# Kernel optimization log

Hardware: AMD Instinct MI355X
Metric: run time of the kernel (lower is better)

## Reference

```python
import jax, jax.numpy as jnp
import numpy as np

N_NODES = 50000


def _gcn_norm(edge_index, num_nodes):
    # PyG gcn_norm with add_self_loops=True, edge_weight=1
    loops = jnp.arange(num_nodes, dtype=edge_index.dtype)
    src = jnp.concatenate([edge_index[0], loops])
    dst = jnp.concatenate([edge_index[1], loops])
    deg = jax.ops.segment_sum(jnp.ones_like(dst, dtype=jnp.float32), dst,
                              num_segments=num_nodes)
    deg_inv_sqrt = jnp.where(deg > 0, jax.lax.rsqrt(jnp.maximum(deg, 1.0)), 0.0)
    norm = deg_inv_sqrt[src] * deg_inv_sqrt[dst]  # [E + N]
    return src, dst, norm


def _gcn_conv(x, src, dst, norm, W, b, num_nodes):
    h = x @ W                                 # [N, out] dense transform first
    msg = h[src] * norm[:, None]              # gather + scale, [E+N, out]
    out = jax.ops.segment_sum(msg, dst, num_segments=num_nodes)  # scatter-add
    return out + b


def setup_inputs() -> dict:
    key = jax.random.key(0)
    k1, k2, k3, k4, k5 = jax.random.split(key, 5)
    in_ch, out_ch = 128, 64
    hid = 2 * out_ch
    x = jax.random.normal(k1, (N_NODES, in_ch), dtype=jnp.float32)
    edge_index = jax.random.randint(k2, (2, 800000), 0, N_NODES, dtype=jnp.int64)
    # Glorot init like PyG GCNConv
    W1 = jax.random.normal(k3, (in_ch, hid), dtype=jnp.float32) * (1.0 / np.sqrt(in_ch))
    b1 = jnp.zeros((hid,), dtype=jnp.float32)
    W2 = jax.random.normal(k4, (hid, out_ch), dtype=jnp.float32) * (1.0 / np.sqrt(hid))
    b2 = jnp.zeros((out_ch,), dtype=jnp.float32)
    return {"x": x, "edge_index": edge_index, "W1": W1, "b1": b1,
            "W2": W2, "b2": b2}


def reference(x, edge_index, W1, b1, W2, b2):
    num_nodes = x.shape[0]
    src, dst, norm = _gcn_norm(edge_index, num_nodes)
    h = _gcn_conv(x, src, dst, norm, W1, b1, num_nodes)
    h = jax.nn.relu(h)
    return _gcn_conv(h, src, dst, norm, W2, b2, num_nodes)
```

## Files before the change

kernel.cpp:

```cpp
#include <hip/hip_runtime.h>

#define N_NODES 50000
#define N_EDGES 800000
#define IN_CH   128
#define HID     128
#define OUT_CH  64

#define NBUCK 196
#define BCAP  5120
#define XPAD  136

#define G1_BLOCKS ((N_NODES + 63) / 64)
#define GSPLIT 391

typedef __attribute__((ext_vector_type(8))) short bf16x8;
typedef __attribute__((ext_vector_type(4))) float f32x4;
typedef unsigned short ushort_t;

__device__ __forceinline__ unsigned short f2bf(float f) {
    unsigned u = __float_as_uint(f);
    u += 0x7fffu + ((u >> 16) & 1u);
    return (unsigned short)(u >> 16);
}
__device__ __forceinline__ unsigned pack2(float a, float b) {
    return (unsigned)f2bf(a) | ((unsigned)f2bf(b) << 16);
}
__device__ __forceinline__ float bf_lo(unsigned u) { return __uint_as_float(u << 16); }
__device__ __forceinline__ float bf_hi(unsigned u) { return __uint_as_float(u & 0xffff0000u); }


__global__ __launch_bounds__(256) void k_prep(const float* __restrict__ W1,
                                              const float* __restrict__ W2,
                                              ushort_t* __restrict__ W1t,
                                              ushort_t* __restrict__ W2t,
                                              int* __restrict__ bcur) {
    if (blockIdx.x == 0 && threadIdx.x < NBUCK) bcur[threadIdx.x] = 0;
    int i = blockIdx.x * 256 + threadIdx.x;
    if (i < 128 * 128) {
        int k = i >> 7, c = i & 127;
        W1t[c * 128 + k] = f2bf(W1[k * 128 + c]);
    } else {
        int j = i - 128 * 128;
        if (j < 128 * 64) {
            int k = j >> 6, c = j & 63;
            W2t[c * 128 + k] = f2bf(W2[k * 64 + c]);
        }
    }
}


__global__ __launch_bounds__(256) void k_stage(const int phase, const int tile0,
                                               const int* __restrict__ src,
                                               const int* __restrict__ dst,
                                               int* __restrict__ bcur,
                                               unsigned* __restrict__ rec,
                                               const float* __restrict__ x,
                                               const ushort_t* __restrict__ W1t,
                                               ushort_t* __restrict__ g,
                                               int* __restrict__ row_beg,
                                               int* __restrict__ row_end,
                                               float* __restrict__ dis,
                                               int* __restrict__ col) {
    __shared__ char smem[52224];
    const int tid = threadIdx.x;

    if (blockIdx.x < NBUCK) {
        if (phase == 0) {
            int* cnt  = (int*)smem;
            int* boff = cnt + 256;
            int* gdel = boff + 256;
            int* bid  = gdel + 256;
            unsigned* stage = (unsigned*)(bid + 4096);

            const int base = blockIdx.x * 4096;
            const int nval = min(4096, N_EDGES - base);

            int dreg[16];
#pragma unroll
            for (int k = 0; k < 16; ++k) {
                int e = base + k * 256 + tid;
                dreg[k] = (e < N_EDGES) ? dst[e] : -1;
            }
            cnt[tid] = 0;
            __syncthreads();
#pragma unroll
            for (int k = 0; k < 16; ++k)
                if (dreg[k] >= 0) atomicAdd(&cnt[dreg[k] >> 8], 1);
            __syncthreads();
            int* s = bid;
            int c = cnt[tid];
            s[tid] = c;
            __syncthreads();
            for (int off = 1; off < 256; off <<= 1) {
                int u = (tid >= off) ? s[tid - off] : 0;
                __syncthreads();
                s[tid] += u;
                __syncthreads();
            }
            boff[tid] = s[tid] - c;
            if (tid < NBUCK && c > 0)
                gdel[tid] = tid * BCAP + atomicAdd(&bcur[tid], c) - boff[tid];
            __syncthreads();
            cnt[tid] = 0;
            __syncthreads();
#pragma unroll
            for (int k = 0; k < 16; ++k) {
                int e = base + k * 256 + tid;
                if (dreg[k] >= 0) {
                    int b = dreg[k] >> 8;
                    int rk = atomicAdd(&cnt[b], 1);
                    int p = boff[b] + rk;
                    stage[p] = (unsigned)src[e] | ((unsigned)(dreg[k] & 255) << 16);
                    bid[p] = b;
                }
            }
            __syncthreads();
            for (int i = tid; i < nval; i += 256) {
                int b = bid[i];
                int p = i + gdel[b];
                if (p < (b + 1) * BCAP)
                    rec[p] = stage[i];
            }
        } else {
            int* hist = (int*)smem;
            int* sbuf = hist + 256;
            int* cur  = sbuf + 256;
            unsigned* stage = (unsigned*)(cur + 256);
            const int b = blockIdx.x;
            const int lo = b * BCAP;
            const int cnt = min(bcur[b], BCAP);

            hist[tid] = 0;
            __syncthreads();
            for (int j = tid; j < cnt; j += 256)
                atomicAdd(&hist[rec[lo + j] >> 16], 1);
            __syncthreads();
            int deg = hist[tid];
            sbuf[tid] = deg;
            __syncthreads();
            for (int off = 1; off < 256; off <<= 1) {
                int u = (tid >= off) ? sbuf[tid - off] : 0;
                __syncthreads();
                sbuf[tid] += u;
                __syncthreads();
            }
            int lbeg = sbuf[tid] - deg;
            int node = (b << 8) + tid;
            if (node < N_NODES) {
                row_beg[node] = lo + lbeg;
                row_end[node] = lo + lbeg + deg;
                dis[node] = rsqrtf((float)deg + 1.0f);
            }
            cur[tid] = lbeg;
            __syncthreads();
            for (int j = tid; j < cnt; j += 256) {
                unsigned r = rec[lo + j];
                int rk = atomicAdd(&cur[r >> 16], 1);
                stage[rk] = r & 0xffffu;
            }
            __syncthreads();
            for (int i = tid; i < cnt; i += 256)
                col[lo + i] = (int)stage[i];
        }
    } else {
        ushort_t* xs = (ushort_t*)smem;
        ushort_t* ws = (ushort_t*)(smem + 17408);
        const int bid = tile0 + (blockIdx.x - NBUCK);
        const int row0 = bid * 64;

        for (int i = tid; i < 64 * 32; i += 256) {
            int r = i >> 5, k4 = (i & 31) << 2;
            int gr = row0 + r;
            float4 v = make_float4(0.f, 0.f, 0.f, 0.f);
            if (gr < N_NODES) v = *(const float4*)&x[(long)gr * IN_CH + k4];
            ushort4 u;
            u.x = f2bf(v.x); u.y = f2bf(v.y); u.z = f2bf(v.z); u.w = f2bf(v.w);
            *(ushort4*)&xs[r * XPAD + k4] = u;
        }
        for (int i = tid; i < 128 * 16; i += 256) {
            int c = i >> 4, seg = i & 15;
            *(uint4*)&ws[c * XPAD + seg * 8] = *(const uint4*)&W1t[c * 128 + seg * 8];
        }
        __syncthreads();

        const int w = tid >> 6, lane = tid & 63;
        const int m = lane & 15, q = lane >> 4;
        const ushort_t* arow = &xs[(w * 16 + m) * XPAD + q * 8];
        const ushort_t* brow = &ws[m * XPAD + q * 8];

        f32x4 acc[8] = {};
#pragma unroll
        for (int k0 = 0; k0 < 128; k0 += 32) {
            bf16x8 a = *(const bf16x8*)(arow + k0);
#pragma unroll
            for (int nt = 0; nt < 8; ++nt) {
                bf16x8 b = *(const bf16x8*)(brow + nt * 16 * XPAD + k0);
                acc[nt] = __builtin_amdgcn_mfma_f32_16x16x32_bf16(a, b, acc[nt], 0, 0, 0);
            }
        }

#pragma unroll
        for (int reg = 0; reg < 4; ++reg) {
            int gr = row0 + w * 16 + q * 4 + reg;
            if (gr < N_NODES) {
#pragma unroll
                for (int nt = 0; nt < 8; ++nt)
                    g[(long)gr * HID + nt * 16 + m] = f2bf(acc[nt][reg]);
            }
        }
    }
}


__global__ __launch_bounds__(256) void k_agg1g2(const int* __restrict__ row_beg,
                                                const int* __restrict__ row_end,
                                                const int* __restrict__ col,
                                                const float* __restrict__ dis,
                                                const ushort_t* __restrict__ g1,
                                                const float* __restrict__ b1,
                                                const ushort_t* __restrict__ W2t,
                                                ushort_t* __restrict__ g3) {
    __shared__ ushort_t hs[16 * XPAD];
    const int tid = threadIdx.x;
    const int w = tid >> 6, lane = tid & 63;
    const int q = lane >> 4;
    const int seg = lane & 15;
    const int cl = seg << 3;
    const uint4* G = (const uint4*)g1;
    const int r0 = blockIdx.x * 16;

    for (int rr = 0; rr < 4; ++rr) {
        const int r = r0 + w * 4 + rr;
        const int beg = row_beg[r], end = row_end[r];

        float acc[8] = {};
        int e = beg + q;
        for (; e + 4 < end; e += 8) {
            int s0 = col[e], s1 = col[e + 4];
            float d0 = dis[s0], d1 = dis[s1];
            uint4 u0 = G[(long)s0 * 16 + seg];
            uint4 u1 = G[(long)s1 * 16 + seg];
            acc[0] += bf_lo(u0.x) * d0; acc[1] += bf_hi(u0.x) * d0;
            acc[2] += bf_lo(u0.y) * d0; acc[3] += bf_hi(u0.y) * d0;
            acc[4] += bf_lo(u0.z) * d0; acc[5] += bf_hi(u0.z) * d0;
            acc[6] += bf_lo(u0.w) * d0; acc[7] += bf_hi(u0.w) * d0;
            acc[0] += bf_lo(u1.x) * d1; acc[1] += bf_hi(u1.x) * d1;
            acc[2] += bf_lo(u1.y) * d1; acc[3] += bf_hi(u1.y) * d1;
            acc[4] += bf_lo(u1.z) * d1; acc[5] += bf_hi(u1.z) * d1;
            acc[6] += bf_lo(u1.w) * d1; acc[7] += bf_hi(u1.w) * d1;
        }
        if (e < end) {
            int s0 = col[e];
            float d0 = dis[s0];
            uint4 u = G[(long)s0 * 16 + seg];
            acc[0] += bf_lo(u.x) * d0; acc[1] += bf_hi(u.x) * d0;
            acc[2] += bf_lo(u.y) * d0; acc[3] += bf_hi(u.y) * d0;
            acc[4] += bf_lo(u.z) * d0; acc[5] += bf_hi(u.z) * d0;
            acc[6] += bf_lo(u.w) * d0; acc[7] += bf_hi(u.w) * d0;
        }
#pragma unroll
        for (int off = 16; off < 64; off <<= 1)
#pragma unroll
            for (int j = 0; j < 8; ++j) acc[j] += __shfl_xor(acc[j], off);

        if (q == 0) {
            const float d = dis[r];
            uint4 u = G[(long)r * 16 + seg];
            acc[0] += bf_lo(u.x) * d; acc[1] += bf_hi(u.x) * d;
            acc[2] += bf_lo(u.y) * d; acc[3] += bf_hi(u.y) * d;
            acc[4] += bf_lo(u.z) * d; acc[5] += bf_hi(u.z) * d;
            acc[6] += bf_lo(u.w) * d; acc[7] += bf_hi(u.w) * d;
            float o[8];
#pragma unroll
            for (int j = 0; j < 8; ++j) o[j] = fmaxf(acc[j] * d + b1[cl + j], 0.f);
            uint4 pw;
            pw.x = pack2(o[0], o[1]); pw.y = pack2(o[2], o[3]);
            pw.z = pack2(o[4], o[5]); pw.w = pack2(o[6], o[7]);
            *(uint4*)&hs[(w * 4 + rr) * XPAD + cl] = pw;
        }
    }
    __syncthreads();

    const int m = lane & 15;
    const ushort_t* arow = &hs[m * XPAD + q * 8];
    const ushort_t* brow = &W2t[(w * 16 + m) * 128 + q * 8];

    f32x4 acc2 = {};
#pragma unroll
    for (int k0 = 0; k0 < 128; k0 += 32) {
        bf16x8 a = *(const bf16x8*)(arow + k0);
        bf16x8 b = *(const bf16x8*)(brow + k0);
        acc2 = __builtin_amdgcn_mfma_f32_16x16x32_bf16(a, b, acc2, 0, 0, 0);
    }

#pragma unroll
    for (int reg = 0; reg < 4; ++reg) {
        int gr = r0 + q * 4 + reg;
        float d = dis[gr];
        g3[(long)gr * OUT_CH + w * 16 + m] = f2bf(acc2[reg] * d);
    }
}


__global__ __launch_bounds__(256) void k_agg2(const int* __restrict__ row_beg,
                                              const int* __restrict__ row_end,
                                              const int* __restrict__ col,
                                              const float* __restrict__ dis,
                                              const ushort_t* __restrict__ g3,
                                              const float* __restrict__ b2,
                                              float* __restrict__ out) {
    int r = blockIdx.x * 4 + (threadIdx.x >> 6);
    if (r >= N_NODES) return;
    const int lane = threadIdx.x & 63;
    const int q = lane >> 3;
    const int seg = lane & 7;
    const int cl = seg << 3;
    const uint4* G = (const uint4*)g3;
    const int beg = row_beg[r], end = row_end[r];

    float acc[8] = {};
    int e = beg + q;
    for (; e + 8 < end; e += 16) {
        int s0 = col[e], s1 = col[e + 8];
        uint4 u0 = G[(long)s0 * 8 + seg];
        uint4 u1 = G[(long)s1 * 8 + seg];
        acc[0] += bf_lo(u0.x); acc[1] += bf_hi(u0.x);
        acc[2] += bf_lo(u0.y); acc[3] += bf_hi(u0.y);
        acc[4] += bf_lo(u0.z); acc[5] += bf_hi(u0.z);
        acc[6] += bf_lo(u0.w); acc[7] += bf_hi(u0.w);
        acc[0] += bf_lo(u1.x); acc[1] += bf_hi(u1.x);
        acc[2] += bf_lo(u1.y); acc[3] += bf_hi(u1.y);
        acc[4] += bf_lo(u1.z); acc[5] += bf_hi(u1.z);
        acc[6] += bf_lo(u1.w); acc[7] += bf_hi(u1.w);
    }
    if (e < end) {
        int s = col[e];
        uint4 u = G[(long)s * 8 + seg];
        acc[0] += bf_lo(u.x); acc[1] += bf_hi(u.x);
        acc[2] += bf_lo(u.y); acc[3] += bf_hi(u.y);
        acc[4] += bf_lo(u.z); acc[5] += bf_hi(u.z);
        acc[6] += bf_lo(u.w); acc[7] += bf_hi(u.w);
    }
#pragma unroll
    for (int off = 8; off < 64; off <<= 1)
#pragma unroll
        for (int j = 0; j < 8; ++j) acc[j] += __shfl_xor(acc[j], off);

    if (q == 0) {
        uint4 u = G[(long)r * 8 + seg];
        acc[0] += bf_lo(u.x); acc[1] += bf_hi(u.x);
        acc[2] += bf_lo(u.y); acc[3] += bf_hi(u.y);
        acc[4] += bf_lo(u.z); acc[5] += bf_hi(u.z);
        acc[6] += bf_lo(u.w); acc[7] += bf_hi(u.w);
        const float d = dis[r];
        float4 o0, o1;
        o0.x = acc[0] * d + b2[cl + 0];
        o0.y = acc[1] * d + b2[cl + 1];
        o0.z = acc[2] * d + b2[cl + 2];
        o0.w = acc[3] * d + b2[cl + 3];
        o1.x = acc[4] * d + b2[cl + 4];
        o1.y = acc[5] * d + b2[cl + 5];
        o1.z = acc[6] * d + b2[cl + 6];
        o1.w = acc[7] * d + b2[cl + 7];
        *(float4*)&out[(long)r * OUT_CH + cl] = o0;
        *(float4*)&out[(long)r * OUT_CH + cl + 4] = o1;
    }
}


extern "C" void kernel_launch(void* const* d_in, const int* in_sizes, int n_in,
                              void* d_out, int out_size, void* d_ws, size_t ws_size,
                              hipStream_t stream) {
    const float* x   = (const float*)d_in[0];
    const int*   ei  = (const int*)d_in[1];
    const float* W1  = (const float*)d_in[2];
    const float* b1  = (const float*)d_in[3];
    const float* W2  = (const float*)d_in[4];
    const float* b2  = (const float*)d_in[5];
    float* out = (float*)d_out;

    const int* src = ei;
    const int* dst = ei + N_EDGES;

    char* p = (char*)d_ws;
    unsigned* rec = (unsigned*)p;         p += (long)NBUCK * BCAP * 4;
    int* col     = (int*)p;               p += (long)NBUCK * BCAP * 4;
    int* row_beg = (int*)p;               p += 50048 * 4;
    int* row_end = (int*)p;               p += 50048 * 4;
    int* bcur    = (int*)p;               p += 256 * 4;
    float* dis   = (float*)p;             p += 50048 * 4;
    ushort_t* W1t = (ushort_t*)p;         p += 128 * 128 * 2;
    ushort_t* W2t = (ushort_t*)p;         p += 128 * 64 * 2;
    ushort_t* g1  = (ushort_t*)p;         p += (long)N_NODES * HID * 2;
    ushort_t* g3  = (ushort_t*)p;

    const int B = 256;

    k_prep<<<96, B, 0, stream>>>(W1, W2, W1t, W2t, bcur);
    k_stage<<<NBUCK + GSPLIT, B, 0, stream>>>(0, 0, src, dst, bcur, rec,
                                              x, W1t, g1, row_beg, row_end, dis, col);
    k_stage<<<NBUCK + (G1_BLOCKS - GSPLIT), B, 0, stream>>>(1, GSPLIT, src, dst, bcur, rec,
                                              x, W1t, g1, row_beg, row_end, dis, col);
    k_agg1g2<<<3125, B, 0, stream>>>(row_beg, row_end, col, dis, g1, b1, W2t, g3);
    k_agg2<<<(N_NODES + 3) / 4, B, 0, stream>>>(row_beg, row_end, col, dis, g3, b2, out);
}
```

Baseline: 173.0 us.

## Split staged kernel into separate scatter, CSR and GEMM kernels; prescale rows by dis

```diff
diff --git a/kernel.cpp b/kernel.cpp
--- a/kernel.cpp
+++ b/kernel.cpp
@@ -10,8 +10,8 @@
 #define BCAP  5120
 #define XPAD  136
 
-#define G1_BLOCKS ((N_NODES + 63) / 64)
-#define GSPLIT 391
+#define SC_BLOCKS 391
+#define SC_EPB    2048
 
 typedef __attribute__((ext_vector_type(8))) short bf16x8;
 typedef __attribute__((ext_vector_type(4))) float f32x4;
@@ -49,164 +49,175 @@
 }
 
 
-__global__ __launch_bounds__(256) void k_stage(const int phase, const int tile0,
-                                               const int* __restrict__ src,
-                                               const int* __restrict__ dst,
-                                               int* __restrict__ bcur,
-                                               unsigned* __restrict__ rec,
-                                               const float* __restrict__ x,
+__global__ __launch_bounds__(256) void k_conv(const float* __restrict__ x,
+                                              ushort_t* __restrict__ xb) {
+    long i = (long)(blockIdx.x * 256 + threadIdx.x) * 8;
+    float4 a = *(const float4*)&x[i];
+    float4 b = *(const float4*)&x[i + 4];
+    ushort_t o[8];
+    o[0] = f2bf(a.x); o[1] = f2bf(a.y); o[2] = f2bf(a.z); o[3] = f2bf(a.w);
+    o[4] = f2bf(b.x); o[5] = f2bf(b.y); o[6] = f2bf(b.z); o[7] = f2bf(b.w);
+    *(uint4*)&xb[i] = *(uint4*)o;
+}
+
+
+__global__ __launch_bounds__(256) void k_scatter(const int* __restrict__ src,
+                                                 const int* __restrict__ dst,
+                                                 int* __restrict__ bcur,
+                                                 unsigned* __restrict__ rec) {
+    __shared__ int cnt[256];
+    __shared__ int boff[256];
+    __shared__ int gdel[256];
+    __shared__ int bid[SC_EPB];
+    __shared__ unsigned stage[SC_EPB];
+    const int tid = threadIdx.x;
+    const int base = blockIdx.x * SC_EPB;
+    const int nval = min(SC_EPB, N_EDGES - base);
+
+    int dreg[8];
+#pragma unroll
+    for (int k = 0; k < 8; ++k) {
+        int e = base + k * 256 + tid;
+        dreg[k] = (e < N_EDGES) ? dst[e] : -1;
+    }
+    cnt[tid] = 0;
+    __syncthreads();
+#pragma unroll
+    for (int k = 0; k < 8; ++k)
+        if (dreg[k] >= 0) atomicAdd(&cnt[dreg[k] >> 8], 1);
+    __syncthreads();
+    int* s = bid;
+    int c = cnt[tid];
+    s[tid] = c;
+    __syncthreads();
+    for (int off = 1; off < 256; off <<= 1) {
+        int u = (tid >= off) ? s[tid - off] : 0;
+        __syncthreads();
+        s[tid] += u;
+        __syncthreads();
+    }
+    boff[tid] = s[tid] - c;
+    if (tid < NBUCK && c > 0)
+        gdel[tid] = tid * BCAP + atomicAdd(&bcur[tid], c) - boff[tid];
+    __syncthreads();
+    cnt[tid] = 0;
+    __syncthreads();
+#pragma unroll
+    for (int k = 0; k < 8; ++k) {
+        int e = base + k * 256 + tid;
+        if (dreg[k] >= 0) {
+            int b = dreg[k] >> 8;
+            int rk = atomicAdd(&cnt[b], 1);
+            int p = boff[b] + rk;
+            stage[p] = (unsigned)src[e] | ((unsigned)(dreg[k] & 255) << 16);
+            bid[p] = b;
+        }
+    }
+    __syncthreads();
+    for (int i = tid; i < nval; i += 256) {
+        int b = bid[i];
+        int p = i + gdel[b];
+        if (p < (b + 1) * BCAP)
+            rec[p] = stage[i];
+    }
+}
+
+
+__global__ __launch_bounds__(256) void k_csr(const int* __restrict__ bcur,
+                                             const unsigned* __restrict__ rec,
+                                             int* __restrict__ row_beg,
+                                             int* __restrict__ row_end,
+                                             float* __restrict__ dis,
+                                             int* __restrict__ col) {
+    __shared__ int hist[256];
+    __shared__ int sbuf[256];
+    __shared__ int cur[256];
+    __shared__ unsigned stage[BCAP];
+    const int tid = threadIdx.x;
+    const int b = blockIdx.x;
+    const int lo = b * BCAP;
+    const int cnt = min(bcur[b], BCAP);
+
+    hist[tid] = 0;
+    __syncthreads();
+    for (int j = tid; j < cnt; j += 256)
+        atomicAdd(&hist[rec[lo + j] >> 16], 1);
+    __syncthreads();
+    int deg = hist[tid];
+    sbuf[tid] = deg;
+    __syncthreads();
+    for (int off = 1; off < 256; off <<= 1) {
+        int u = (tid >= off) ? sbuf[tid - off] : 0;
+        __syncthreads();
+        sbuf[tid] += u;
+        __syncthreads();
+    }
+    int lbeg = sbuf[tid] - deg;
+    int node = (b << 8) + tid;
+    if (node < N_NODES) {
+        row_beg[node] = lo + lbeg;
+        row_end[node] = lo + lbeg + deg;
+        dis[node] = rsqrtf((float)deg + 1.0f);
+    }
+    cur[tid] = lbeg;
+    __syncthreads();
+    for (int j = tid; j < cnt; j += 256) {
+        unsigned r = rec[lo + j];
+        int rk = atomicAdd(&cur[r >> 16], 1);
+        stage[rk] = r & 0xffffu;
+    }
+    __syncthreads();
+    for (int i = tid; i < cnt; i += 256)
+        col[lo + i] = (int)stage[i];
+}
+
+
+__global__ __launch_bounds__(256) void k_gemm1(const ushort_t* __restrict__ xb,
                                                const ushort_t* __restrict__ W1t,
-                                               ushort_t* __restrict__ g,
-                                               int* __restrict__ row_beg,
-                                               int* __restrict__ row_end,
-                                               float* __restrict__ dis,
-                                               int* __restrict__ col) {
-    __shared__ char smem[52224];
+                                               const float* __restrict__ dis,
+                                               ushort_t* __restrict__ g1) {
+    __shared__ ushort_t xs[64 * XPAD];
+    __shared__ ushort_t ws[128 * XPAD];
     const int tid = threadIdx.x;
-
-    if (blockIdx.x < NBUCK) {
-        if (phase == 0) {
-            int* cnt  = (int*)smem;
-            int* boff = cnt + 256;
-            int* gdel = boff + 256;
-            int* bid  = gdel + 256;
-            unsigned* stage = (unsigned*)(bid + 4096);
-
-            const int base = blockIdx.x * 4096;
-            const int nval = min(4096, N_EDGES - base);
-
-            int dreg[16];
-#pragma unroll
-            for (int k = 0; k < 16; ++k) {
-                int e = base + k * 256 + tid;
-                dreg[k] = (e < N_EDGES) ? dst[e] : -1;
-            }
-            cnt[tid] = 0;
-            __syncthreads();
-#pragma unroll
-            for (int k = 0; k < 16; ++k)
-                if (dreg[k] >= 0) atomicAdd(&cnt[dreg[k] >> 8], 1);
-            __syncthreads();
-            int* s = bid;
-            int c = cnt[tid];
-            s[tid] = c;
-            __syncthreads();
-            for (int off = 1; off < 256; off <<= 1) {
-                int u = (tid >= off) ? s[tid - off] : 0;
-                __syncthreads();
-                s[tid] += u;
-                __syncthreads();
-            }
-            boff[tid] = s[tid] - c;
-            if (tid < NBUCK && c > 0)
-                gdel[tid] = tid * BCAP + atomicAdd(&bcur[tid], c) - boff[tid];
-            __syncthreads();
-            cnt[tid] = 0;
-            __syncthreads();
-#pragma unroll
-            for (int k = 0; k < 16; ++k) {
-                int e = base + k * 256 + tid;
-                if (dreg[k] >= 0) {
-                    int b = dreg[k] >> 8;
-                    int rk = atomicAdd(&cnt[b], 1);
-                    int p = boff[b] + rk;
-                    stage[p] = (unsigned)src[e] | ((unsigned)(dreg[k] & 255) << 16);
-                    bid[p] = b;
-                }
-            }
-            __syncthreads();
-            for (int i = tid; i < nval; i += 256) {
-                int b = bid[i];
-                int p = i + gdel[b];
-                if (p < (b + 1) * BCAP)
-                    rec[p] = stage[i];
-            }
-        } else {
-            int* hist = (int*)smem;
-            int* sbuf = hist + 256;
-            int* cur  = sbuf + 256;
-            unsigned* stage = (unsigned*)(cur + 256);
-            const int b = blockIdx.x;
-            const int lo = b * BCAP;
-            const int cnt = min(bcur[b], BCAP);
-
-            hist[tid] = 0;
-            __syncthreads();
-            for (int j = tid; j < cnt; j += 256)
-                atomicAdd(&hist[rec[lo + j] >> 16], 1);
-            __syncthreads();
-            int deg = hist[tid];
-            sbuf[tid] = deg;
-            __syncthreads();
-            for (int off = 1; off < 256; off <<= 1) {
-                int u = (tid >= off) ? sbuf[tid - off] : 0;
-                __syncthreads();
-                sbuf[tid] += u;
-                __syncthreads();
-            }
-            int lbeg = sbuf[tid] - deg;
-            int node = (b << 8) + tid;
-            if (node < N_NODES) {
-                row_beg[node] = lo + lbeg;
-                row_end[node] = lo + lbeg + deg;
-                dis[node] = rsqrtf((float)deg + 1.0f);
-            }
-            cur[tid] = lbeg;
-            __syncthreads();
-            for (int j = tid; j < cnt; j += 256) {
-                unsigned r = rec[lo + j];
-                int rk = atomicAdd(&cur[r >> 16], 1);
-                stage[rk] = r & 0xffffu;
-            }
-            __syncthreads();
-            for (int i = tid; i < cnt; i += 256)
-                col[lo + i] = (int)stage[i];
-        }
-    } else {
-        ushort_t* xs = (ushort_t*)smem;
-        ushort_t* ws = (ushort_t*)(smem + 17408);
-        const int bid = tile0 + (blockIdx.x - NBUCK);
-        const int row0 = bid * 64;
-
-        for (int i = tid; i < 64 * 32; i += 256) {
-            int r = i >> 5, k4 = (i & 31) << 2;
-            int gr = row0 + r;
-            float4 v = make_float4(0.f, 0.f, 0.f, 0.f);
-            if (gr < N_NODES) v = *(const float4*)&x[(long)gr * IN_CH + k4];
-            ushort4 u;
-            u.x = f2bf(v.x); u.y = f2bf(v.y); u.z = f2bf(v.z); u.w = f2bf(v.w);
-            *(ushort4*)&xs[r * XPAD + k4] = u;
-        }
-        for (int i = tid; i < 128 * 16; i += 256) {
-            int c = i >> 4, seg = i & 15;
-            *(uint4*)&ws[c * XPAD + seg * 8] = *(const uint4*)&W1t[c * 128 + seg * 8];
-        }
-        __syncthreads();
-
-        const int w = tid >> 6, lane = tid & 63;
-        const int m = lane & 15, q = lane >> 4;
-        const ushort_t* arow = &xs[(w * 16 + m) * XPAD + q * 8];
-        const ushort_t* brow = &ws[m * XPAD + q * 8];
-
-        f32x4 acc[8] = {};
-#pragma unroll
-        for (int k0 = 0; k0 < 128; k0 += 32) {
-            bf16x8 a = *(const bf16x8*)(arow + k0);
-#pragma unroll
-            for (int nt = 0; nt < 8; ++nt) {
-                bf16x8 b = *(const bf16x8*)(brow + nt * 16 * XPAD + k0);
-                acc[nt] = __builtin_amdgcn_mfma_f32_16x16x32_bf16(a, b, acc[nt], 0, 0, 0);
-            }
-        }
-
-#pragma unroll
-        for (int reg = 0; reg < 4; ++reg) {
-            int gr = row0 + w * 16 + q * 4 + reg;
-            if (gr < N_NODES) {
-#pragma unroll
-                for (int nt = 0; nt < 8; ++nt)
-                    g[(long)gr * HID + nt * 16 + m] = f2bf(acc[nt][reg]);
-            }
+    const int row0 = blockIdx.x * 64;
+
+    for (int i = tid; i < 64 * 16; i += 256) {
+        int r = i >> 4, seg = i & 15;
+        int gr = row0 + r;
+        uint4 v = make_uint4(0u, 0u, 0u, 0u);
+        if (gr < N_NODES) v = *(const uint4*)&xb[(long)gr * IN_CH + seg * 8];
+        *(uint4*)&xs[r * XPAD + seg * 8] = v;
+    }
+    for (int i = tid; i < 128 * 16; i += 256) {
+        int c = i >> 4, seg = i & 15;
+        *(uint4*)&ws[c * XPAD + seg * 8] = *(const uint4*)&W1t[c * 128 + seg * 8];
+    }
+    __syncthreads();
+
+    const int w = tid >> 6, lane = tid & 63;
+    const int m = lane & 15, q = lane >> 4;
+    const ushort_t* arow = &xs[(w * 16 + m) * XPAD + q * 8];
+    const ushort_t* brow = &ws[m * XPAD + q * 8];
+
+    f32x4 acc[8] = {};
+#pragma unroll
+    for (int k0 = 0; k0 < 128; k0 += 32) {
+        bf16x8 a = *(const bf16x8*)(arow + k0);
+#pragma unroll
+        for (int nt = 0; nt < 8; ++nt) {
+            bf16x8 b = *(const bf16x8*)(brow + nt * 16 * XPAD + k0);
+            acc[nt] = __builtin_amdgcn_mfma_f32_16x16x32_bf16(a, b, acc[nt], 0, 0, 0);
+        }
+    }
+
+#pragma unroll
+    for (int reg = 0; reg < 4; ++reg) {
+        int gr = row0 + w * 16 + q * 4 + reg;
+        if (gr < N_NODES) {
+            float d = dis[gr];
+#pragma unroll
+            for (int nt = 0; nt < 8; ++nt)
+                g1[(long)gr * HID + nt * 16 + m] = f2bf(acc[nt][reg] * d);
         }
     }
 }
@@ -237,26 +248,24 @@
         int e = beg + q;
         for (; e + 4 < end; e += 8) {
             int s0 = col[e], s1 = col[e + 4];
-            float d0 = dis[s0], d1 = dis[s1];
             uint4 u0 = G[(long)s0 * 16 + seg];
             uint4 u1 = G[(long)s1 * 16 + seg];
-            acc[0] += bf_lo(u0.x) * d0; acc[1] += bf_hi(u0.x) * d0;
-            acc[2] += bf_lo(u0.y) * d0; acc[3] += bf_hi(u0.y) * d0;
-            acc[4] += bf_lo(u0.z) * d0; acc[5] += bf_hi(u0.z) * d0;
-            acc[6] += bf_lo(u0.w) * d0; acc[7] += bf_hi(u0.w) * d0;
-            acc[0] += bf_lo(u1.x) * d1; acc[1] += bf_hi(u1.x) * d1;
-            acc[2] += bf_lo(u1.y) * d1; acc[3] += bf_hi(u1.y) * d1;
-            acc[4] += bf_lo(u1.z) * d1; acc[5] += bf_hi(u1.z) * d1;
-            acc[6] += bf_lo(u1.w) * d1; acc[7] += bf_hi(u1.w) * d1;
+            acc[0] += bf_lo(u0.x); acc[1] += bf_hi(u0.x);
+            acc[2] += bf_lo(u0.y); acc[3] += bf_hi(u0.y);
+            acc[4] += bf_lo(u0.z); acc[5] += bf_hi(u0.z);
+            acc[6] += bf_lo(u0.w); acc[7] += bf_hi(u0.w);
+            acc[0] += bf_lo(u1.x); acc[1] += bf_hi(u1.x);
+            acc[2] += bf_lo(u1.y); acc[3] += bf_hi(u1.y);
+            acc[4] += bf_lo(u1.z); acc[5] += bf_hi(u1.z);
+            acc[6] += bf_lo(u1.w); acc[7] += bf_hi(u1.w);
         }
         if (e < end) {
             int s0 = col[e];
-            float d0 = dis[s0];
             uint4 u = G[(long)s0 * 16 + seg];
-            acc[0] += bf_lo(u.x) * d0; acc[1] += bf_hi(u.x) * d0;
-            acc[2] += bf_lo(u.y) * d0; acc[3] += bf_hi(u.y) * d0;
-            acc[4] += bf_lo(u.z) * d0; acc[5] += bf_hi(u.z) * d0;
-            acc[6] += bf_lo(u.w) * d0; acc[7] += bf_hi(u.w) * d0;
+            acc[0] += bf_lo(u.x); acc[1] += bf_hi(u.x);
+            acc[2] += bf_lo(u.y); acc[3] += bf_hi(u.y);
+            acc[4] += bf_lo(u.z); acc[5] += bf_hi(u.z);
+            acc[6] += bf_lo(u.w); acc[7] += bf_hi(u.w);
         }
 #pragma unroll
         for (int off = 16; off < 64; off <<= 1)
@@ -264,12 +273,12 @@
             for (int j = 0; j < 8; ++j) acc[j] += __shfl_xor(acc[j], off);
 
         if (q == 0) {
+            uint4 u = G[(long)r * 16 + seg];
+            acc[0] += bf_lo(u.x); acc[1] += bf_hi(u.x);
+            acc[2] += bf_lo(u.y); acc[3] += bf_hi(u.y);
+            acc[4] += bf_lo(u.z); acc[5] += bf_hi(u.z);
+            acc[6] += bf_lo(u.w); acc[7] += bf_hi(u.w);
             const float d = dis[r];
-            uint4 u = G[(long)r * 16 + seg];
-            acc[0] += bf_lo(u.x) * d; acc[1] += bf_hi(u.x) * d;
-            acc[2] += bf_lo(u.y) * d; acc[3] += bf_hi(u.y) * d;
-            acc[4] += bf_lo(u.z) * d; acc[5] += bf_hi(u.z) * d;
-            acc[6] += bf_lo(u.w) * d; acc[7] += bf_hi(u.w) * d;
             float o[8];
 #pragma unroll
             for (int j = 0; j < 8; ++j) o[j] = fmaxf(acc[j] * d + b1[cl + j], 0.f);
@@ -391,16 +400,17 @@
     float* dis   = (float*)p;             p += 50048 * 4;
     ushort_t* W1t = (ushort_t*)p;         p += 128 * 128 * 2;
     ushort_t* W2t = (ushort_t*)p;         p += 128 * 64 * 2;
+    ushort_t* xb  = (ushort_t*)p;         p += (long)N_NODES * IN_CH * 2;
     ushort_t* g1  = (ushort_t*)p;         p += (long)N_NODES * HID * 2;
     ushort_t* g3  = (ushort_t*)p;
 
     const int B = 256;
 
     k_prep<<<96, B, 0, stream>>>(W1, W2, W1t, W2t, bcur);
-    k_stage<<<NBUCK + GSPLIT, B, 0, stream>>>(0, 0, src, dst, bcur, rec,
-                                              x, W1t, g1, row_beg, row_end, dis, col);
-    k_stage<<<NBUCK + (G1_BLOCKS - GSPLIT), B, 0, stream>>>(1, GSPLIT, src, dst, bcur, rec,
-                                              x, W1t, g1, row_beg, row_end, dis, col);
+    k_conv<<<3125, B, 0, stream>>>(x, xb);
+    k_scatter<<<SC_BLOCKS, B, 0, stream>>>(src, dst, bcur, rec);
+    k_csr<<<NBUCK, B, 0, stream>>>(bcur, rec, row_beg, row_end, dis, col);
+    k_gemm1<<<(N_NODES + 63) / 64, B, 0, stream>>>(xb, W1t, dis, g1);
     k_agg1g2<<<3125, B, 0, stream>>>(row_beg, row_end, col, dis, g1, b1, W2t, g3);
     k_agg2<<<(N_NODES + 3) / 4, B, 0, stream>>>(row_beg, row_end, col, dis, g3, b2, out);
 }
```

Result: slower. 182.5 us (+5.5%).

## Split feature matrices into 32-channel planes for cache-local gathers; unfuse GEMM2

Applied to the files above, without the earlier changes.

```diff
diff --git a/kernel.cpp b/kernel.cpp
--- a/kernel.cpp
+++ b/kernel.cpp
@@ -12,6 +12,9 @@
 
 #define G1_BLOCKS ((N_NODES + 63) / 64)
 #define GSPLIT 391
+
+#define PLANE (N_NODES * 32)
+#define NROWB 3125
 
 typedef __attribute__((ext_vector_type(8))) short bf16x8;
 typedef __attribute__((ext_vector_type(4))) float f32x4;
@@ -56,7 +59,7 @@
                                                unsigned* __restrict__ rec,
                                                const float* __restrict__ x,
                                                const ushort_t* __restrict__ W1t,
-                                               ushort_t* __restrict__ g,
+                                               ushort_t* __restrict__ g1q,
                                                int* __restrict__ row_beg,
                                                int* __restrict__ row_end,
                                                float* __restrict__ dis,
@@ -205,99 +208,118 @@
             if (gr < N_NODES) {
 #pragma unroll
                 for (int nt = 0; nt < 8; ++nt)
-                    g[(long)gr * HID + nt * 16 + m] = f2bf(acc[nt][reg]);
-            }
-        }
-    }
-}
-
-
-__global__ __launch_bounds__(256) void k_agg1g2(const int* __restrict__ row_beg,
-                                                const int* __restrict__ row_end,
-                                                const int* __restrict__ col,
-                                                const float* __restrict__ dis,
-                                                const ushort_t* __restrict__ g1,
-                                                const float* __restrict__ b1,
-                                                const ushort_t* __restrict__ W2t,
-                                                ushort_t* __restrict__ g3) {
-    __shared__ ushort_t hs[16 * XPAD];
+                    g1q[(long)(nt >> 1) * PLANE + gr * 32 + (nt & 1) * 16 + m]
+                        = f2bf(acc[nt][reg]);
+            }
+        }
+    }
+}
+
+
+__global__ __launch_bounds__(256) void k_agg1(const int* __restrict__ row_beg,
+                                              const int* __restrict__ row_end,
+                                              const int* __restrict__ col,
+                                              const float* __restrict__ dis,
+                                              const ushort_t* __restrict__ g1q,
+                                              const float* __restrict__ b1,
+                                              ushort_t* __restrict__ a1q) {
+    const int qq = blockIdx.x / NROWB;
+    const int nb = blockIdx.x % NROWB;
     const int tid = threadIdx.x;
     const int w = tid >> 6, lane = tid & 63;
-    const int q = lane >> 4;
-    const int seg = lane & 15;
-    const int cl = seg << 3;
-    const uint4* G = (const uint4*)g1;
-    const int r0 = blockIdx.x * 16;
+    const int es = lane >> 2;
+    const int seg = lane & 3;
+    const uint4* G = (const uint4*)(g1q + (long)qq * PLANE);
+    const int r0 = nb * 16;
 
     for (int rr = 0; rr < 4; ++rr) {
         const int r = r0 + w * 4 + rr;
         const int beg = row_beg[r], end = row_end[r];
 
         float acc[8] = {};
-        int e = beg + q;
-        for (; e + 4 < end; e += 8) {
-            int s0 = col[e], s1 = col[e + 4];
-            float d0 = dis[s0], d1 = dis[s1];
-            uint4 u0 = G[(long)s0 * 16 + seg];
-            uint4 u1 = G[(long)s1 * 16 + seg];
-            acc[0] += bf_lo(u0.x) * d0; acc[1] += bf_hi(u0.x) * d0;
-            acc[2] += bf_lo(u0.y) * d0; acc[3] += bf_hi(u0.y) * d0;
-            acc[4] += bf_lo(u0.z) * d0; acc[5] += bf_hi(u0.z) * d0;
-            acc[6] += bf_lo(u0.w) * d0; acc[7] += bf_hi(u0.w) * d0;
-            acc[0] += bf_lo(u1.x) * d1; acc[1] += bf_hi(u1.x) * d1;
-            acc[2] += bf_lo(u1.y) * d1; acc[3] += bf_hi(u1.y) * d1;
-            acc[4] += bf_lo(u1.z) * d1; acc[5] += bf_hi(u1.z) * d1;
-            acc[6] += bf_lo(u1.w) * d1; acc[7] += bf_hi(u1.w) * d1;
-        }
-        if (e < end) {
-            int s0 = col[e];
-            float d0 = dis[s0];
-            uint4 u = G[(long)s0 * 16 + seg];
-            acc[0] += bf_lo(u.x) * d0; acc[1] += bf_hi(u.x) * d0;
-            acc[2] += bf_lo(u.y) * d0; acc[3] += bf_hi(u.y) * d0;
-            acc[4] += bf_lo(u.z) * d0; acc[5] += bf_hi(u.z) * d0;
-            acc[6] += bf_lo(u.w) * d0; acc[7] += bf_hi(u.w) * d0;
-        }
-#pragma unroll
-        for (int off = 16; off < 64; off <<= 1)
+        for (int e = beg + es; e < end; e += 16) {
+            int s = col[e];
+            float d = dis[s];
+            uint4 u = G[s * 4 + seg];
+            acc[0] += bf_lo(u.x) * d; acc[1] += bf_hi(u.x) * d;
+            acc[2] += bf_lo(u.y) * d; acc[3] += bf_hi(u.y) * d;
+            acc[4] += bf_lo(u.z) * d; acc[5] += bf_hi(u.z) * d;
+            acc[6] += bf_lo(u.w) * d; acc[7] += bf_hi(u.w) * d;
+        }
+#pragma unroll
+        for (int off = 4; off < 64; off <<= 1)
 #pragma unroll
             for (int j = 0; j < 8; ++j) acc[j] += __shfl_xor(acc[j], off);
 
-        if (q == 0) {
+        if (es == 0) {
             const float d = dis[r];
-            uint4 u = G[(long)r * 16 + seg];
+            uint4 u = G[r * 4 + seg];
             acc[0] += bf_lo(u.x) * d; acc[1] += bf_hi(u.x) * d;
             acc[2] += bf_lo(u.y) * d; acc[3] += bf_hi(u.y) * d;
             acc[4] += bf_lo(u.z) * d; acc[5] += bf_hi(u.z) * d;
             acc[6] += bf_lo(u.w) * d; acc[7] += bf_hi(u.w) * d;
             float o[8];
 #pragma unroll
-            for (int j = 0; j < 8; ++j) o[j] = fmaxf(acc[j] * d + b1[cl + j], 0.f);
+            for (int j = 0; j < 8; ++j)
+                o[j] = fmaxf(acc[j] * d + b1[qq * 32 + seg * 8 + j], 0.f);
             uint4 pw;
             pw.x = pack2(o[0], o[1]); pw.y = pack2(o[2], o[3]);
             pw.z = pack2(o[4], o[5]); pw.w = pack2(o[6], o[7]);
-            *(uint4*)&hs[(w * 4 + rr) * XPAD + cl] = pw;
-        }
+            *(uint4*)&a1q[(long)qq * PLANE + r * 32 + seg * 8] = pw;
+        }
+    }
+}
+
+
+__global__ __launch_bounds__(256) void k_gemm2(const ushort_t* __restrict__ a1q,
+                                               const ushort_t* __restrict__ W2t,
+                                               const float* __restrict__ dis,
+                                               ushort_t* __restrict__ g3h) {
+    __shared__ ushort_t xs[64 * XPAD];
+    __shared__ ushort_t ws[64 * XPAD];
+    const int tid = threadIdx.x;
+    const int row0 = blockIdx.x * 64;
+
+    for (int i = tid; i < 64 * 16; i += 256) {
+        int r = i >> 4, seg = i & 15;
+        int gr = row0 + r;
+        uint4 v = make_uint4(0u, 0u, 0u, 0u);
+        if (gr < N_NODES)
+            v = *(const uint4*)&a1q[(long)(seg >> 2) * PLANE + gr * 32 + (seg & 3) * 8];
+        *(uint4*)&xs[r * XPAD + seg * 8] = v;
+    }
+    for (int i = tid; i < 64 * 16; i += 256) {
+        int c = i >> 4, seg = i & 15;
+        *(uint4*)&ws[c * XPAD + seg * 8] = *(const uint4*)&W2t[c * 128 + seg * 8];
     }
     __syncthreads();
 
-    const int m = lane & 15;
-    const ushort_t* arow = &hs[m * XPAD + q * 8];
-    const ushort_t* brow = &W2t[(w * 16 + m) * 128 + q * 8];
-
-    f32x4 acc2 = {};
+    const int w = tid >> 6, lane = tid & 63;
+    const int m = lane & 15, q = lane >> 4;
+    const ushort_t* arow = &xs[(w * 16 + m) * XPAD + q * 8];
+    const ushort_t* brow = &ws[m * XPAD + q * 8];
+
+    f32x4 acc[4] = {};
 #pragma unroll
     for (int k0 = 0; k0 < 128; k0 += 32) {
         bf16x8 a = *(const bf16x8*)(arow + k0);
-        bf16x8 b = *(const bf16x8*)(brow + k0);
-        acc2 = __builtin_amdgcn_mfma_f32_16x16x32_bf16(a, b, acc2, 0, 0, 0);
+#pragma unroll
+        for (int nt = 0; nt < 4; ++nt) {
+            bf16x8 b = *(const bf16x8*)(brow + nt * 16 * XPAD + k0);
+            acc[nt] = __builtin_amdgcn_mfma_f32_16x16x32_bf16(a, b, acc[nt], 0, 0, 0);
+        }
     }
 
 #pragma unroll
     for (int reg = 0; reg < 4; ++reg) {
-        int gr = r0 + q * 4 + reg;
-        float d = dis[gr];
-        g3[(long)gr * OUT_CH + w * 16 + m] = f2bf(acc2[reg] * d);
+        int gr = row0 + w * 16 + q * 4 + reg;
+        if (gr < N_NODES) {
+            float d = dis[gr];
+#pragma unroll
+            for (int nt = 0; nt < 4; ++nt)
+                g3h[(long)(nt >> 1) * PLANE + gr * 32 + (nt & 1) * 16 + m]
+                    = f2bf(acc[nt][reg] * d);
+        }
     }
 }
 
@@ -306,64 +328,56 @@
                                               const int* __restrict__ row_end,
                                               const int* __restrict__ col,
                                               const float* __restrict__ dis,
-                                              const ushort_t* __restrict__ g3,
+                                              const ushort_t* __restrict__ g3h,
                                               const float* __restrict__ b2,
                                               float* __restrict__ out) {
-    int r = blockIdx.x * 4 + (threadIdx.x >> 6);
-    if (r >= N_NODES) return;
-    const int lane = threadIdx.x & 63;
-    const int q = lane >> 3;
-    const int seg = lane & 7;
-    const int cl = seg << 3;
-    const uint4* G = (const uint4*)g3;
-    const int beg = row_beg[r], end = row_end[r];
-
-    float acc[8] = {};
-    int e = beg + q;
-    for (; e + 8 < end; e += 16) {
-        int s0 = col[e], s1 = col[e + 8];
-        uint4 u0 = G[(long)s0 * 8 + seg];
-        uint4 u1 = G[(long)s1 * 8 + seg];
-        acc[0] += bf_lo(u0.x); acc[1] += bf_hi(u0.x);
-        acc[2] += bf_lo(u0.y); acc[3] += bf_hi(u0.y);
-        acc[4] += bf_lo(u0.z); acc[5] += bf_hi(u0.z);
-        acc[6] += bf_lo(u0.w); acc[7] += bf_hi(u0.w);
-        acc[0] += bf_lo(u1.x); acc[1] += bf_hi(u1.x);
-        acc[2] += bf_lo(u1.y); acc[3] += bf_hi(u1.y);
-        acc[4] += bf_lo(u1.z); acc[5] += bf_hi(u1.z);
-        acc[6] += bf_lo(u1.w); acc[7] += bf_hi(u1.w);
-    }
-    if (e < end) {
-        int s = col[e];
-        uint4 u = G[(long)s * 8 + seg];
-        acc[0] += bf_lo(u.x); acc[1] += bf_hi(u.x);
-        acc[2] += bf_lo(u.y); acc[3] += bf_hi(u.y);
-        acc[4] += bf_lo(u.z); acc[5] += bf_hi(u.z);
-        acc[6] += bf_lo(u.w); acc[7] += bf_hi(u.w);
-    }
-#pragma unroll
-    for (int off = 8; off < 64; off <<= 1)
-#pragma unroll
-        for (int j = 0; j < 8; ++j) acc[j] += __shfl_xor(acc[j], off);
-
-    if (q == 0) {
-        uint4 u = G[(long)r * 8 + seg];
-        acc[0] += bf_lo(u.x); acc[1] += bf_hi(u.x);
-        acc[2] += bf_lo(u.y); acc[3] += bf_hi(u.y);
-        acc[4] += bf_lo(u.z); acc[5] += bf_hi(u.z);
-        acc[6] += bf_lo(u.w); acc[7] += bf_hi(u.w);
-        const float d = dis[r];
-        float4 o0, o1;
-        o0.x = acc[0] * d + b2[cl + 0];
-        o0.y = acc[1] * d + b2[cl + 1];
-        o0.z = acc[2] * d + b2[cl + 2];
-        o0.w = acc[3] * d + b2[cl + 3];
-        o1.x = acc[4] * d + b2[cl + 4];
-        o1.y = acc[5] * d + b2[cl + 5];
-        o1.z = acc[6] * d + b2[cl + 6];
-        o1.w = acc[7] * d + b2[cl + 7];
-        *(float4*)&out[(long)r * OUT_CH + cl] = o0;
-        *(float4*)&out[(long)r * OUT_CH + cl + 4] = o1;
+    const int hh = blockIdx.x / NROWB;
+    const int nb = blockIdx.x % NROWB;
+    const int tid = threadIdx.x;
+    const int w = tid >> 6, lane = tid & 63;
+    const int es = lane >> 2;
+    const int seg = lane & 3;
+    const uint4* G = (const uint4*)(g3h + (long)hh * PLANE);
+    const int r0 = nb * 16;
+
+    for (int rr = 0; rr < 4; ++rr) {
+        const int r = r0 + w * 4 + rr;
+        const int beg = row_beg[r], end = row_end[r];
+
+        float acc[8] = {};
+        for (int e = beg + es; e < end; e += 16) {
+            int s = col[e];
+            uint4 u = G[s * 4 + seg];
+            acc[0] += bf_lo(u.x); acc[1] += bf_hi(u.x);
+            acc[2] += bf_lo(u.y); acc[3] += bf_hi(u.y);
+            acc[4] += bf_lo(u.z); acc[5] += bf_hi(u.z);
+            acc[6] += bf_lo(u.w); acc[7] += bf_hi(u.w);
+        }
+#pragma unroll
+        for (int off = 4; off < 64; off <<= 1)
+#pragma unroll
+            for (int j = 0; j < 8; ++j) acc[j] += __shfl_xor(acc[j], off);
+
+        if (es == 0) {
+            uint4 u = G[r * 4 + seg];
+            acc[0] += bf_lo(u.x); acc[1] += bf_hi(u.x);
+            acc[2] += bf_lo(u.y); acc[3] += bf_hi(u.y);
+            acc[4] += bf_lo(u.z); acc[5] += bf_hi(u.z);
+            acc[6] += bf_lo(u.w); acc[7] += bf_hi(u.w);
+            const float d = dis[r];
+            float4 o0, o1;
+            const int cb = hh * 32 + seg * 8;
+            o0.x = acc[0] * d + b2[cb + 0];
+            o0.y = acc[1] * d + b2[cb + 1];
+            o0.z = acc[2] * d + b2[cb + 2];
+            o0.w = acc[3] * d + b2[cb + 3];
+            o1.x = acc[4] * d + b2[cb + 4];
+            o1.y = acc[5] * d + b2[cb + 5];
+            o1.z = acc[6] * d + b2[cb + 6];
+            o1.w = acc[7] * d + b2[cb + 7];
+            *(float4*)&out[(long)r * OUT_CH + cb] = o0;
+            *(float4*)&out[(long)r * OUT_CH + cb + 4] = o1;
+        }
     }
 }
 
@@ -391,16 +405,18 @@
     float* dis   = (float*)p;             p += 50048 * 4;
     ushort_t* W1t = (ushort_t*)p;         p += 128 * 128 * 2;
     ushort_t* W2t = (ushort_t*)p;         p += 128 * 64 * 2;
-    ushort_t* g1  = (ushort_t*)p;         p += (long)N_NODES * HID * 2;
-    ushort_t* g3  = (ushort_t*)p;
+    ushort_t* g1q = (ushort_t*)p;         p += (long)4 * PLANE * 2;
+    ushort_t* a1q = (ushort_t*)p;         p += (long)4 * PLANE * 2;
+    ushort_t* g3h = (ushort_t*)p;
 
     const int B = 256;
 
     k_prep<<<96, B, 0, stream>>>(W1, W2, W1t, W2t, bcur);
     k_stage<<<NBUCK + GSPLIT, B, 0, stream>>>(0, 0, src, dst, bcur, rec,
-                                              x, W1t, g1, row_beg, row_end, dis, col);
+                                              x, W1t, g1q, row_beg, row_end, dis, col);
     k_stage<<<NBUCK + (G1_BLOCKS - GSPLIT), B, 0, stream>>>(1, GSPLIT, src, dst, bcur, rec,
-                                              x, W1t, g1, row_beg, row_end, dis, col);
-    k_agg1g2<<<3125, B, 0, stream>>>(row_beg, row_end, col, dis, g1, b1, W2t, g3);
-    k_agg2<<<(N_NODES + 3) / 4, B, 0, stream>>>(row_beg, row_end, col, dis, g3, b2, out);
-}
+                                              x, W1t, g1q, row_beg, row_end, dis, col);
+    k_agg1<<<4 * NROWB, B, 0, stream>>>(row_beg, row_end, col, dis, g1q, b1, a1q);
+    k_gemm2<<<(N_NODES + 63) / 64, B, 0, stream>>>(a1q, W2t, dis, g3h);
+    k_agg2<<<2 * NROWB, B, 0, stream>>>(row_beg, row_end, col, dis, g3h, b2, out);
+}
```

After: 226.5 us. +31.0%, slower.

## Split fused stage kernel into separate GEMM, scatter and CSR kernels with 1024-thread blocks

Applied to the files above, without the earlier changes.

```diff
diff --git a/kernel.cpp b/kernel.cpp
--- a/kernel.cpp
+++ b/kernel.cpp
@@ -9,9 +9,6 @@
 #define NBUCK 196
 #define BCAP  5120
 #define XPAD  136
-
-#define G1_BLOCKS ((N_NODES + 63) / 64)
-#define GSPLIT 391
 
 typedef __attribute__((ext_vector_type(8))) short bf16x8;
 typedef __attribute__((ext_vector_type(4))) float f32x4;
@@ -49,166 +46,170 @@
 }
 
 
-__global__ __launch_bounds__(256) void k_stage(const int phase, const int tile0,
-                                               const int* __restrict__ src,
-                                               const int* __restrict__ dst,
-                                               int* __restrict__ bcur,
-                                               unsigned* __restrict__ rec,
-                                               const float* __restrict__ x,
-                                               const ushort_t* __restrict__ W1t,
-                                               ushort_t* __restrict__ g,
-                                               int* __restrict__ row_beg,
-                                               int* __restrict__ row_end,
-                                               float* __restrict__ dis,
-                                               int* __restrict__ col) {
-    __shared__ char smem[52224];
+__global__ __launch_bounds__(256) void k_g1(const float* __restrict__ x,
+                                            const ushort_t* __restrict__ W1t,
+                                            ushort_t* __restrict__ g1) {
+    __shared__ ushort_t xs[64 * XPAD];
+    __shared__ ushort_t ws[128 * XPAD];
     const int tid = threadIdx.x;
-
-    if (blockIdx.x < NBUCK) {
-        if (phase == 0) {
-            int* cnt  = (int*)smem;
-            int* boff = cnt + 256;
-            int* gdel = boff + 256;
-            int* bid  = gdel + 256;
-            unsigned* stage = (unsigned*)(bid + 4096);
-
-            const int base = blockIdx.x * 4096;
-            const int nval = min(4096, N_EDGES - base);
-
-            int dreg[16];
-#pragma unroll
-            for (int k = 0; k < 16; ++k) {
-                int e = base + k * 256 + tid;
-                dreg[k] = (e < N_EDGES) ? dst[e] : -1;
-            }
-            cnt[tid] = 0;
-            __syncthreads();
-#pragma unroll
-            for (int k = 0; k < 16; ++k)
-                if (dreg[k] >= 0) atomicAdd(&cnt[dreg[k] >> 8], 1);
-            __syncthreads();
-            int* s = bid;
-            int c = cnt[tid];
-            s[tid] = c;
-            __syncthreads();
-            for (int off = 1; off < 256; off <<= 1) {
-                int u = (tid >= off) ? s[tid - off] : 0;
-                __syncthreads();
-                s[tid] += u;
-                __syncthreads();
-            }
-            boff[tid] = s[tid] - c;
-            if (tid < NBUCK && c > 0)
-                gdel[tid] = tid * BCAP + atomicAdd(&bcur[tid], c) - boff[tid];
-            __syncthreads();
-            cnt[tid] = 0;
-            __syncthreads();
-#pragma unroll
-            for (int k = 0; k < 16; ++k) {
-                int e = base + k * 256 + tid;
-                if (dreg[k] >= 0) {
-                    int b = dreg[k] >> 8;
-                    int rk = atomicAdd(&cnt[b], 1);
-                    int p = boff[b] + rk;
-                    stage[p] = (unsigned)src[e] | ((unsigned)(dreg[k] & 255) << 16);
-                    bid[p] = b;
-                }
-            }
-            __syncthreads();
-            for (int i = tid; i < nval; i += 256) {
-                int b = bid[i];
-                int p = i + gdel[b];
-                if (p < (b + 1) * BCAP)
-                    rec[p] = stage[i];
-            }
-        } else {
-            int* hist = (int*)smem;
-            int* sbuf = hist + 256;
-            int* cur  = sbuf + 256;
-            unsigned* stage = (unsigned*)(cur + 256);
-            const int b = blockIdx.x;
-            const int lo = b * BCAP;
-            const int cnt = min(bcur[b], BCAP);
-
-            hist[tid] = 0;
-            __syncthreads();
-            for (int j = tid; j < cnt; j += 256)
-                atomicAdd(&hist[rec[lo + j] >> 16], 1);
-            __syncthreads();
-            int deg = hist[tid];
-            sbuf[tid] = deg;
-            __syncthreads();
-            for (int off = 1; off < 256; off <<= 1) {
-                int u = (tid >= off) ? sbuf[tid - off] : 0;
-                __syncthreads();
-                sbuf[tid] += u;
-                __syncthreads();
-            }
-            int lbeg = sbuf[tid] - deg;
-            int node = (b << 8) + tid;
-            if (node < N_NODES) {
-                row_beg[node] = lo + lbeg;
-                row_end[node] = lo + lbeg + deg;
-                dis[node] = rsqrtf((float)deg + 1.0f);
-            }
-            cur[tid] = lbeg;
-            __syncthreads();
-            for (int j = tid; j < cnt; j += 256) {
-                unsigned r = rec[lo + j];
-                int rk = atomicAdd(&cur[r >> 16], 1);
-                stage[rk] = r & 0xffffu;
-            }
-            __syncthreads();
-            for (int i = tid; i < cnt; i += 256)
-                col[lo + i] = (int)stage[i];
-        }
-    } else {
-        ushort_t* xs = (ushort_t*)smem;
-        ushort_t* ws = (ushort_t*)(smem + 17408);
-        const int bid = tile0 + (blockIdx.x - NBUCK);
-        const int row0 = bid * 64;
-
-        for (int i = tid; i < 64 * 32; i += 256) {
-            int r = i >> 5, k4 = (i & 31) << 2;
-            int gr = row0 + r;
-            float4 v = make_float4(0.f, 0.f, 0.f, 0.f);
-            if (gr < N_NODES) v = *(const float4*)&x[(long)gr * IN_CH + k4];
-            ushort4 u;
-            u.x = f2bf(v.x); u.y = f2bf(v.y); u.z = f2bf(v.z); u.w = f2bf(v.w);
-            *(ushort4*)&xs[r * XPAD + k4] = u;
-        }
-        for (int i = tid; i < 128 * 16; i += 256) {
-            int c = i >> 4, seg = i & 15;
-            *(uint4*)&ws[c * XPAD + seg * 8] = *(const uint4*)&W1t[c * 128 + seg * 8];
-        }
+    const int row0 = blockIdx.x * 64;
+
+    for (int i = tid; i < 64 * 32; i += 256) {
+        int r = i >> 5, k4 = (i & 31) << 2;
+        int gr = row0 + r;
+        float4 v = make_float4(0.f, 0.f, 0.f, 0.f);
+        if (gr < N_NODES) v = *(const float4*)&x[(long)gr * IN_CH + k4];
+        ushort4 u;
+        u.x = f2bf(v.x); u.y = f2bf(v.y); u.z = f2bf(v.z); u.w = f2bf(v.w);
+        *(ushort4*)&xs[r * XPAD + k4] = u;
+    }
+    for (int i = tid; i < 128 * 16; i += 256) {
+        int c = i >> 4, seg = i & 15;
+        *(uint4*)&ws[c * XPAD + seg * 8] = *(const uint4*)&W1t[c * 128 + seg * 8];
+    }
+    __syncthreads();
+
+    const int w = tid >> 6, lane = tid & 63;
+    const int m = lane & 15, q = lane >> 4;
+    const ushort_t* arow = &xs[(w * 16 + m) * XPAD + q * 8];
+    const ushort_t* brow = &ws[m * XPAD + q * 8];
+
+    f32x4 acc[8] = {};
+#pragma unroll
+    for (int k0 = 0; k0 < 128; k0 += 32) {
+        bf16x8 a = *(const bf16x8*)(arow + k0);
+#pragma unroll
+        for (int nt = 0; nt < 8; ++nt) {
+            bf16x8 b = *(const bf16x8*)(brow + nt * 16 * XPAD + k0);
+            acc[nt] = __builtin_amdgcn_mfma_f32_16x16x32_bf16(a, b, acc[nt], 0, 0, 0);
+        }
+    }
+
+#pragma unroll
+    for (int reg = 0; reg < 4; ++reg) {
+        int gr = row0 + w * 16 + q * 4 + reg;
+        if (gr < N_NODES) {
+#pragma unroll
+            for (int nt = 0; nt < 8; ++nt)
+                g1[(long)gr * HID + nt * 16 + m] = f2bf(acc[nt][reg]);
+        }
+    }
+}
+
+
+__global__ __launch_bounds__(1024) void k_sc(const int* __restrict__ src,
+                                             const int* __restrict__ dst,
+                                             int* __restrict__ bcur,
+                                             unsigned* __restrict__ rec) {
+    __shared__ int cnt[256];
+    __shared__ int boff[256];
+    __shared__ int gdel[256];
+    __shared__ int bid[4096];
+    __shared__ unsigned stage[4096];
+    const int tid = threadIdx.x;
+    const int base = blockIdx.x * 4096;
+    const int nval = min(4096, N_EDGES - base);
+
+    int dreg[4];
+#pragma unroll
+    for (int k = 0; k < 4; ++k) {
+        int e = base + k * 1024 + tid;
+        dreg[k] = (e < N_EDGES) ? dst[e] : -1;
+    }
+    if (tid < 256) cnt[tid] = 0;
+    __syncthreads();
+#pragma unroll
+    for (int k = 0; k < 4; ++k)
+        if (dreg[k] >= 0) atomicAdd(&cnt[dreg[k] >> 8], 1);
+    __syncthreads();
+    int c = 0;
+    if (tid < 256) { c = cnt[tid]; bid[tid] = c; }
+    __syncthreads();
+    for (int off = 1; off < 256; off <<= 1) {
+        int u = 0;
+        if (tid < 256 && tid >= off) u = bid[tid - off];
         __syncthreads();
-
-        const int w = tid >> 6, lane = tid & 63;
-        const int m = lane & 15, q = lane >> 4;
-        const ushort_t* arow = &xs[(w * 16 + m) * XPAD + q * 8];
-        const ushort_t* brow = &ws[m * XPAD + q * 8];
-
-        f32x4 acc[8] = {};
-#pragma unroll
-        for (int k0 = 0; k0 < 128; k0 += 32) {
-            bf16x8 a = *(const bf16x8*)(arow + k0);
-#pragma unroll
-            for (int nt = 0; nt < 8; ++nt) {
-                bf16x8 b = *(const bf16x8*)(brow + nt * 16 * XPAD + k0);
-                acc[nt] = __builtin_amdgcn_mfma_f32_16x16x32_bf16(a, b, acc[nt], 0, 0, 0);
-            }
-        }
-
-#pragma unroll
-        for (int reg = 0; reg < 4; ++reg) {
-            int gr = row0 + w * 16 + q * 4 + reg;
-            if (gr < N_NODES) {
-#pragma unroll
-                for (int nt = 0; nt < 8; ++nt)
-                    g[(long)gr * HID + nt * 16 + m] = f2bf(acc[nt][reg]);
-            }
-        }
-    }
+        if (tid < 256) bid[tid] += u;
+        __syncthreads();
+    }
+    if (tid < 256) {
+        boff[tid] = bid[tid] - c;
+        gdel[tid] = 0;
+        if (tid < NBUCK && c > 0)
+            gdel[tid] = tid * BCAP + atomicAdd(&bcur[tid], c) - boff[tid];
+        cnt[tid] = 0;
+    }
+    __syncthreads();
+#pragma unroll
+    for (int k = 0; k < 4; ++k) {
+        int e = base + k * 1024 + tid;
+        if (dreg[k] >= 0) {
+            int b = dreg[k] >> 8;
+            int rk = atomicAdd(&cnt[b], 1);
+            int p = boff[b] + rk;
+            stage[p] = (unsigned)src[e] | ((unsigned)(dreg[k] & 255) << 16);
+            bid[p] = b;
+        }
+    }
+    __syncthreads();
+    for (int i = tid; i < nval; i += 1024) {
+        int b = bid[i];
+        int p = i + gdel[b];
+        if (p < (b + 1) * BCAP)
+            rec[p] = stage[i];
+    }
+}
+
+
+__global__ __launch_bounds__(1024) void k_csr(const int* __restrict__ bcur,
+                                              const unsigned* __restrict__ rec,
+                                              int* __restrict__ row_beg,
+                                              int* __restrict__ row_end,
+                                              float* __restrict__ dis,
+                                              int* __restrict__ col) {
+    __shared__ int hist[256];
+    __shared__ int sbuf[256];
+    __shared__ int cur[256];
+    __shared__ unsigned stage[BCAP];
+    const int tid = threadIdx.x;
+    const int b = blockIdx.x;
+    const int lo = b * BCAP;
+    const int cnt = min(bcur[b], BCAP);
+
+    if (tid < 256) hist[tid] = 0;
+    __syncthreads();
+    for (int j = tid; j < cnt; j += 1024)
+        atomicAdd(&hist[rec[lo + j] >> 16], 1);
+    __syncthreads();
+    if (tid < 256) sbuf[tid] = hist[tid];
+    __syncthreads();
+    for (int off = 1; off < 256; off <<= 1) {
+        int u = 0;
+        if (tid < 256 && tid >= off) u = sbuf[tid - off];
+        __syncthreads();
+        if (tid < 256) sbuf[tid] += u;
+        __syncthreads();
+    }
+    if (tid < 256) {
+        int deg = hist[tid];
+        int lbeg = sbuf[tid] - deg;
+        int node = (b << 8) + tid;
+        if (node < N_NODES) {
+            row_beg[node] = lo + lbeg;
+            row_end[node] = lo + lbeg + deg;
+            dis[node] = rsqrtf((float)deg + 1.0f);
+        }
+        cur[tid] = lbeg;
+    }
+    __syncthreads();
+    for (int j = tid; j < cnt; j += 1024) {
+        unsigned r = rec[lo + j];
+        int rk = atomicAdd(&cur[r >> 16], 1);
+        stage[rk] = r & 0xffffu;
+    }
+    __syncthreads();
+    for (int i = tid; i < cnt; i += 1024)
+        col[lo + i] = (int)stage[i];
 }
 
 
@@ -394,13 +395,10 @@
     ushort_t* g1  = (ushort_t*)p;         p += (long)N_NODES * HID * 2;
     ushort_t* g3  = (ushort_t*)p;
 
-    const int B = 256;
-
-    k_prep<<<96, B, 0, stream>>>(W1, W2, W1t, W2t, bcur);
-    k_stage<<<NBUCK + GSPLIT, B, 0, stream>>>(0, 0, src, dst, bcur, rec,
-                                              x, W1t, g1, row_beg, row_end, dis, col);
-    k_stage<<<NBUCK + (G1_BLOCKS - GSPLIT), B, 0, stream>>>(1, GSPLIT, src, dst, bcur, rec,
-                                              x, W1t, g1, row_beg, row_end, dis, col);
-    k_agg1g2<<<3125, B, 0, stream>>>(row_beg, row_end, col, dis, g1, b1, W2t, g3);
-    k_agg2<<<(N_NODES + 3) / 4, B, 0, stream>>>(row_beg, row_end, col, dis, g3, b2, out);
-}
+    k_prep<<<96, 256, 0, stream>>>(W1, W2, W1t, W2t, bcur);
+    k_g1<<<(N_NODES + 63) / 64, 256, 0, stream>>>(x, W1t, g1);
+    k_sc<<<(N_EDGES + 4095) / 4096, 1024, 0, stream>>>(src, dst, bcur, rec);
+    k_csr<<<NBUCK, 1024, 0, stream>>>(bcur, rec, row_beg, row_end, dis, col);
+    k_agg1g2<<<3125, 256, 0, stream>>>(row_beg, row_end, col, dis, g1, b1, W2t, g3);
+    k_agg2<<<(N_NODES + 3) / 4, 256, 0, stream>>>(row_beg, row_end, col, dis, g3, b2, out);
+}
```

Result: no change. 172.9 us (-0.0%).
